# Optimization experiments

Hardware: AMD Instinct MI355X
Metric: run time of the kernel (lower is better)

Reference implementation:

```python
import jax, jax.numpy as jnp
import numpy as np

UNITS = 1024
B, T = 32, 2048


def setup_inputs() -> dict:
    key = jax.random.key(0)
    ks = jax.random.split(key, 8)
    s = 1.0 / np.sqrt(UNITS)
    return {
        "x": jax.random.normal(ks[0], (B, T, UNITS), dtype=jnp.float32),
        "hidden": jax.random.normal(ks[1], (B, UNITS), dtype=jnp.float32),
        "W1_w": jax.random.uniform(ks[2], (UNITS, UNITS), jnp.float32, -s, s),
        "W1_b": jax.random.uniform(ks[3], (UNITS,), jnp.float32, -s, s),
        "W2_w": jax.random.uniform(ks[4], (UNITS, UNITS), jnp.float32, -s, s),
        "W2_b": jax.random.uniform(ks[5], (UNITS,), jnp.float32, -s, s),
        "V_w": jax.random.uniform(ks[6], (1, UNITS), jnp.float32, -s, s),
        "V_b": jax.random.uniform(ks[7], (1,), jnp.float32, -s, s),
    }


def reference(x, hidden, W1_w, W1_b, W2_w, W2_b, V_w, V_b):
    # hidden.squeeze().unsqueeze(1): [B, U] -> [B, 1, U]
    h = hidden[:, None, :]
    # tanh(W1(x) + W2(hidden)): [B, T, U]
    att = jnp.tanh(
        jnp.einsum("btu,vu->btv", x, W1_w) + W1_b
        + jnp.einsum("bsu,vu->bsv", h, W2_w) + W2_b
    )
    # score = V(att): [B, T, 1]
    score = jnp.einsum("btu,ou->bto", att, V_w) + V_b
    # softmax over T, then squeeze().unsqueeze(1): [B, T, 1] -> [B, 1, T]
    attention_weights = jnp.swapaxes(jax.nn.softmax(score, axis=1), 1, 2)
    # bmm([B,1,T], [B,T,U]) -> [B,1,U]; squeeze().unsqueeze(0) -> [1, B, U]
    context_vector = jnp.matmul(attention_weights, x)[:, 0, :][None, :, :]
    return context_vector, attention_weights
```

## Files before the change

kernel.cpp:

```cpp
#include <hip/hip_runtime.h>
#include <hip/hip_bf16.h>
#include <cstdint>
#include <cstddef>

#define UNITS 1024
#define BDIM 32
#define TDIM 2048
#define M_TOT (BDIM*TDIM)
#define KDIM UNITS
#define NDIM UNITS
#define NPART 4

#define K2LOG2E 2.885390081777927f

typedef __attribute__((ext_vector_type(8))) short bf16x8;
typedef __attribute__((ext_vector_type(8))) unsigned short ushort8;
typedef __attribute__((ext_vector_type(4))) float f32x4;

__device__ __forceinline__ unsigned short f2bf(float f) {
  unsigned u = __float_as_uint(f);
  u += 0x7fffu + ((u >> 16) & 1u);
  return (unsigned short)(u >> 16);
}
__device__ __forceinline__ float bf2f(unsigned short h) {
  return __uint_as_float(((unsigned)h) << 16);
}

__global__ __launch_bounds__(256) void cvt_kernel(const float* __restrict__ src,
                                                  ushort* __restrict__ dst, int n8) {
  int i = blockIdx.x * blockDim.x + threadIdx.x;
  int stride = gridDim.x * blockDim.x;
  const float4* s4 = (const float4*)src;
  ushort8* d8 = (ushort8*)dst;
  for (; i < n8; i += stride) {
    float4 a = s4[2*i], b = s4[2*i+1];
    ushort8 o;
    o[0] = f2bf(a.x); o[1] = f2bf(a.y); o[2] = f2bf(a.z); o[3] = f2bf(a.w);
    o[4] = f2bf(b.x); o[5] = f2bf(b.y); o[6] = f2bf(b.z); o[7] = f2bf(b.w);
    d8[i] = o;
  }
}

__global__ __launch_bounds__(64) void prep_c_kernel(const float* __restrict__ W2w,
                                                    const float* __restrict__ hidden,
                                                    const float* __restrict__ W1b,
                                                    const float* __restrict__ W2b,
                                                    float* __restrict__ c) {
  int v = blockIdx.x;
  int l = threadIdx.x;
  float acc[BDIM];
  #pragma unroll
  for (int b = 0; b < BDIM; b++) acc[b] = 0.f;
  for (int u0 = 0; u0 < UNITS; u0 += 64) {
    float w = W2w[v*UNITS + u0 + l];
    #pragma unroll
    for (int b = 0; b < BDIM; b++) acc[b] += w * hidden[b*UNITS + u0 + l];
  }
  float bias = W1b[v] + W2b[v];
  #pragma unroll
  for (int b = 0; b < BDIM; b++) {
    float s = acc[b];
    #pragma unroll
    for (int off = 32; off > 0; off >>= 1) s += __shfl_xor(s, off);
    if (l == 0) c[b*UNITS + v] = s + bias;
  }
}

#define GLL(g, l) __builtin_amdgcn_global_load_lds(                              \
    (const __attribute__((address_space(1))) void*)(g),                          \
    (__attribute__((address_space(3))) void*)(l), 16, 0, 0)

__global__ __launch_bounds__(512, 2) void gemm_score_kernel(
    const ushort* __restrict__ A,
    const ushort* __restrict__ W,
    const float* __restrict__ c,
    const float* __restrict__ Vw,
    float* __restrict__ score)
{
  __shared__ ushort sh[2][2][16384];
  ushort* shb = &sh[0][0][0];

  const int nt = blockIdx.x & 3;
  const int m0 = (blockIdx.x >> 2) * 256;
  const int n0 = nt * 256;
  const int bb = m0 >> 11;
  const int tid = threadIdx.x;
  const int wave = tid >> 6;
  const int l = tid & 63;
  const int lrow = l & 15;
  const int lq = l >> 4;
  const int wm = (wave >> 2) * 128;
  const int wn = (wave & 3) * 64;

  const int srow = tid >> 3;
  const int s_g  = ((tid & 7) - srow) & 7;
  const int p0 = ((lq + lrow) & 7) * 8;
  const int p1 = ((lq + lrow + 4) & 7) * 8;
  const int aoff = (wm + lrow) * 64;
  const int boff = (wn + lrow) * 64;

  const ushort* gA0 = A + (size_t)(m0 + srow) * KDIM + s_g * 8;
  const ushort* gA1 = gA0 + (size_t)64 * KDIM;
  const ushort* gA2 = gA0 + (size_t)128 * KDIM;
  const ushort* gA3 = gA0 + (size_t)192 * KDIM;
  const ushort* gB0 = W + (size_t)(n0 + srow) * KDIM + s_g * 8;
  const ushort* gB1 = gB0 + (size_t)64 * KDIM;
  const ushort* gB2 = gB0 + (size_t)128 * KDIM;
  const ushort* gB3 = gB0 + (size_t)192 * KDIM;

  f32x4 acc[8][4];
  #pragma unroll
  for (int i = 0; i < 8; i++)
    #pragma unroll
    for (int j = 0; j < 4; j++) acc[i][j] = (f32x4)0.f;

  auto STAGE = [&](int buf) {
    ushort* dA = shb + buf * 32768 + wave * 512;
    ushort* dB = dA + 16384;
    GLL(gA0, dA);          GLL(gA1, dA + 4096);
    GLL(gA2, dA + 8192);   GLL(gA3, dA + 12288);
    GLL(gB0, dB);          GLL(gB1, dB + 4096);
    GLL(gB2, dB + 8192);   GLL(gB3, dB + 12288);
    gA0 += 64; gA1 += 64; gA2 += 64; gA3 += 64;
    gB0 += 64; gB1 += 64; gB2 += 64; gB3 += 64;
  };

  auto COMPUTE = [&](int buf) {
    const ushort* Ab = shb + buf * 32768;
    const ushort* Bb = Ab + 16384;
    {
      bf16x8 a[8], b[4];
      #pragma unroll
      for (int i = 0; i < 8; i++) a[i] = *(const bf16x8*)(Ab + aoff + i * 1024 + p0);
      #pragma unroll
      for (int j = 0; j < 4; j++) b[j] = *(const bf16x8*)(Bb + boff + j * 1024 + p0);
      __builtin_amdgcn_s_setprio(1);
      #pragma unroll
      for (int i = 0; i < 8; i++)
        #pragma unroll
        for (int j = 0; j < 4; j++)
          acc[i][j] = __builtin_amdgcn_mfma_f32_16x16x32_bf16(a[i], b[j], acc[i][j], 0, 0, 0);
      __builtin_amdgcn_s_setprio(0);
    }
    {
      bf16x8 a[8], b[4];
      #pragma unroll
      for (int i = 0; i < 8; i++) a[i] = *(const bf16x8*)(Ab + aoff + i * 1024 + p1);
      #pragma unroll
      for (int j = 0; j < 4; j++) b[j] = *(const bf16x8*)(Bb + boff + j * 1024 + p1);
      __builtin_amdgcn_s_setprio(1);
      #pragma unroll
      for (int i = 0; i < 8; i++)
        #pragma unroll
        for (int j = 0; j < 4; j++)
          acc[i][j] = __builtin_amdgcn_mfma_f32_16x16x32_bf16(a[i], b[j], acc[i][j], 0, 0, 0);
      __builtin_amdgcn_s_setprio(0);
    }
  };

  STAGE(0);
  STAGE(1);
  asm volatile("s_waitcnt vmcnt(8)" ::: "memory");
  __builtin_amdgcn_s_barrier();
  int cur = 0;
  #pragma unroll 1
  for (int kt = 0; kt < 14; ++kt) {
    COMPUTE(cur);
    asm volatile("s_waitcnt lgkmcnt(0)" ::: "memory");
    __builtin_amdgcn_s_barrier();
    STAGE(cur);
    asm volatile("s_waitcnt vmcnt(8)" ::: "memory");
    __builtin_amdgcn_s_barrier();
    cur ^= 1;
  }
  COMPUTE(cur);
  asm volatile("s_waitcnt lgkmcnt(0)" ::: "memory");
  __builtin_amdgcn_s_barrier();
  asm volatile("s_waitcnt vmcnt(0)" ::: "memory");
  __builtin_amdgcn_s_barrier();
  COMPUTE(cur ^ 1);

  float vw4[4], ck4[4];
  float vws = 0.f;
  #pragma unroll
  for (int j = 0; j < 4; j++) {
    int n = n0 + wn + j * 16 + lrow;
    float v = Vw[n];
    vw4[j] = v;
    vws += v;
    ck4[j] = c[bb * NDIM + n] * K2LOG2E;
  }
  float sacc[8][4];
  #pragma unroll
  for (int i = 0; i < 8; i++)
    #pragma unroll
    for (int r = 0; r < 4; r++) sacc[i][r] = 0.f;
  #pragma unroll
  for (int i = 0; i < 8; i++)
    #pragma unroll
    for (int j = 0; j < 4; j++)
      #pragma unroll
      for (int r = 0; r < 4; r++) {
        float t = __builtin_fmaf(acc[i][j][r], K2LOG2E, ck4[j]);
        float e = __builtin_amdgcn_exp2f(t);
        float rr = __builtin_amdgcn_rcpf(e + 1.f);
        sacc[i][r] = __builtin_fmaf(vw4[j], rr, sacc[i][r]);
      }

  float* sred = (float*)shb;
  #pragma unroll
  for (int i = 0; i < 8; i++)
    #pragma unroll
    for (int r = 0; r < 4; r++) {
      float s = vws - 2.f * sacc[i][r];
      s += __shfl_xor(s, 1);
      s += __shfl_xor(s, 2);
      s += __shfl_xor(s, 4);
      s += __shfl_xor(s, 8);
      if (lrow == 0) sred[wave * 128 + i * 16 + lq * 4 + r] = s;
    }
  __syncthreads();
  if (tid < 256) {
    int mh = tid >> 7;
    int ml = tid & 127;
    float v = sred[mh * 512 + ml] + sred[mh * 512 + 128 + ml]
            + sred[mh * 512 + 256 + ml] + sred[mh * 512 + 384 + ml];
    score[(size_t)nt * M_TOT + m0 + tid] = v;
  }
}

__global__ __launch_bounds__(256) void softmax_kernel(float* __restrict__ sc,
                                                      float* __restrict__ wout) {
  const int b = blockIdx.x;
  const int tid = threadIdx.x;
  float4* s4 = (float4*)(sc + (size_t)b * TDIM);
  float4 v0 = s4[2*tid], v1 = s4[2*tid+1];
  #pragma unroll
  for (int k = 1; k < NPART; k++) {
    const float4* p4 = (const float4*)(sc + (size_t)k * M_TOT + (size_t)b * TDIM);
    float4 u0 = p4[2*tid], u1 = p4[2*tid+1];
    v0.x += u0.x; v0.y += u0.y; v0.z += u0.z; v0.w += u0.w;
    v1.x += u1.x; v1.y += u1.y; v1.z += u1.z; v1.w += u1.w;
  }
  float mx = fmaxf(fmaxf(fmaxf(v0.x,v0.y),fmaxf(v0.z,v0.w)),
                   fmaxf(fmaxf(v1.x,v1.y),fmaxf(v1.z,v1.w)));
  #pragma unroll
  for (int off = 32; off > 0; off >>= 1) mx = fmaxf(mx, __shfl_xor(mx, off));
  __shared__ float redm[4];
  __shared__ float reds[4];
  if ((tid & 63) == 0) redm[tid >> 6] = mx;
  __syncthreads();
  mx = fmaxf(fmaxf(redm[0], redm[1]), fmaxf(redm[2], redm[3]));
  v0.x = __expf(v0.x - mx); v0.y = __expf(v0.y - mx);
  v0.z = __expf(v0.z - mx); v0.w = __expf(v0.w - mx);
  v1.x = __expf(v1.x - mx); v1.y = __expf(v1.y - mx);
  v1.z = __expf(v1.z - mx); v1.w = __expf(v1.w - mx);
  float sum = v0.x+v0.y+v0.z+v0.w+v1.x+v1.y+v1.z+v1.w;
  #pragma unroll
  for (int off = 32; off > 0; off >>= 1) sum += __shfl_xor(sum, off);
  if ((tid & 63) == 0) reds[tid >> 6] = sum;
  __syncthreads();
  sum = reds[0]+reds[1]+reds[2]+reds[3];
  float inv = 1.f / sum;
  v0.x *= inv; v0.y *= inv; v0.z *= inv; v0.w *= inv;
  v1.x *= inv; v1.y *= inv; v1.z *= inv; v1.w *= inv;
  s4[2*tid] = v0; s4[2*tid+1] = v1;
  float4* w4 = (float4*)(wout + (size_t)b * TDIM);
  w4[2*tid] = v0; w4[2*tid+1] = v1;
}

__global__ __launch_bounds__(256) void context_kernel(const ushort* __restrict__ xb,
                                                      const float* __restrict__ wgt,
                                                      float* __restrict__ ctx) {
  const int uc = blockIdx.x;
  const int b = blockIdx.y;
  const int tid = threadIdx.x;
  __shared__ float wl[TDIM];
  {
    const float4* wsrc = (const float4*)(wgt + (size_t)b * TDIM);
    float4* wdst = (float4*)wl;
    wdst[tid] = wsrc[tid];
    wdst[tid + 256] = wsrc[tid + 256];
  }
  __syncthreads();
  const int ut = tid & 15;
  const int tr = tid >> 4;
  const ushort* xp = xb + (size_t)b * TDIM * UNITS + uc * 128 + ut * 8;
  float a8[8];
  #pragma unroll
  for (int e = 0; e < 8; e++) a8[e] = 0.f;
  for (int t = tr; t < TDIM; t += 64) {
    ushort8 x0 = *(const ushort8*)(xp + (size_t)(t     ) * UNITS);
    ushort8 x1 = *(const ushort8*)(xp + (size_t)(t + 16) * UNITS);
    ushort8 x2 = *(const ushort8*)(xp + (size_t)(t + 32) * UNITS);
    ushort8 x3 = *(const ushort8*)(xp + (size_t)(t + 48) * UNITS);
    float w0 = wl[t], w1 = wl[t+16], w2 = wl[t+32], w3 = wl[t+48];
    #pragma unroll
    for (int e = 0; e < 8; e++) {
      a8[e] += w0 * bf2f(x0[e]);
      a8[e] += w1 * bf2f(x1[e]);
      a8[e] += w2 * bf2f(x2[e]);
      a8[e] += w3 * bf2f(x3[e]);
    }
  }
  #pragma unroll
  for (int e = 0; e < 8; e++) {
    a8[e] += __shfl_xor(a8[e], 16);
    a8[e] += __shfl_xor(a8[e], 32);
  }
  __shared__ float red[512];
  const int wave = tid >> 6;
  const int l = tid & 63;
  if (l < 16) {
    #pragma unroll
    for (int e = 0; e < 8; e++) red[wave * 128 + l * 8 + e] = a8[e];
  }
  __syncthreads();
  if (tid < 128) {
    float v = red[tid] + red[128 + tid] + red[256 + tid] + red[384 + tid];
    ctx[(size_t)b * UNITS + uc * 128 + tid] = v;
  }
}

extern "C" void kernel_launch(void* const* d_in, const int* in_sizes, int n_in,
                              void* d_out, int out_size, void* d_ws, size_t ws_size,
                              hipStream_t stream) {
  const float* x   = (const float*)d_in[0];
  const float* hid = (const float*)d_in[1];
  const float* W1w = (const float*)d_in[2];
  const float* W1b = (const float*)d_in[3];
  const float* W2w = (const float*)d_in[4];
  const float* W2b = (const float*)d_in[5];
  const float* Vw  = (const float*)d_in[6];
  float* out = (float*)d_out;

  char* ws = (char*)d_ws;
  ushort* xb   = (ushort*)ws;
  ushort* w1b  = (ushort*)(ws + (size_t)M_TOT*KDIM*2);
  float*  cbuf = (float*)(ws + (size_t)M_TOT*KDIM*2 + (size_t)NDIM*KDIM*2);
  float*  score= (float*)((char*)cbuf + (size_t)BDIM*NDIM*4);

  cvt_kernel<<<4096, 256, 0, stream>>>(x, xb, M_TOT*KDIM/8);
  cvt_kernel<<<512, 256, 0, stream>>>(W1w, w1b, NDIM*KDIM/8);
  prep_c_kernel<<<NDIM, 64, 0, stream>>>(W2w, hid, W1b, W2b, cbuf);
  gemm_score_kernel<<<M_TOT/256 * NPART, 512, 0, stream>>>(xb, w1b, cbuf, Vw, score);
  softmax_kernel<<<BDIM, 256, 0, stream>>>(score, out + (size_t)BDIM*UNITS);
  context_kernel<<<dim3(8, BDIM), 256, 0, stream>>>(xb, score, out);
}
```

Measured before the change: 579.0 us.

## Restructure GEMM mainloop into 4-slot K=32 ring with interleaved staging

Replaces the double-buffered K=64 tile pipeline with a four-slot ring of K=32 half-tiles. Each K-step is split into phases that issue async global-to-LDS loads for a future half-tile between the LDS fragment reads and the MFMA block, with per-phase barriers and vmcnt waits. The LDS swizzle is changed to match the 32-wide rows. The goal is finer-grained overlap of memory traffic with MFMA work, at the cost of more barriers per iteration and more intricate wait-count bookkeeping.

```diff
diff --git a/kernel.cpp b/kernel.cpp
--- a/kernel.cpp
+++ b/kernel.cpp
@@ -77,8 +77,7 @@
     const float* __restrict__ Vw,
     float* __restrict__ score)
 {
-  __shared__ ushort sh[2][2][16384];
-  ushort* shb = &sh[0][0][0];
+  __shared__ ushort shb[65536];
 
   const int nt = blockIdx.x & 3;
   const int m0 = (blockIdx.x >> 2) * 256;
@@ -92,21 +91,13 @@
   const int wm = (wave >> 2) * 128;
   const int wn = (wave & 3) * 64;
 
-  const int srow = tid >> 3;
-  const int s_g  = ((tid & 7) - srow) & 7;
-  const int p0 = ((lq + lrow) & 7) * 8;
-  const int p1 = ((lq + lrow + 4) & 7) * 8;
-  const int aoff = (wm + lrow) * 64;
-  const int boff = (wn + lrow) * 64;
-
-  const ushort* gA0 = A + (size_t)(m0 + srow) * KDIM + s_g * 8;
-  const ushort* gA1 = gA0 + (size_t)64 * KDIM;
-  const ushort* gA2 = gA0 + (size_t)128 * KDIM;
-  const ushort* gA3 = gA0 + (size_t)192 * KDIM;
-  const ushort* gB0 = W + (size_t)(n0 + srow) * KDIM + s_g * 8;
-  const ushort* gB1 = gB0 + (size_t)64 * KDIM;
-  const ushort* gB2 = gB0 + (size_t)128 * KDIM;
-  const ushort* gB3 = gB0 + (size_t)192 * KDIM;
+  const int s_g = ((tid & 3) - (tid >> 3)) & 3;
+  const ushort* sA = A + (size_t)(m0 + (tid >> 2)) * KDIM + s_g * 8;
+  const ushort* sB = W + (size_t)(n0 + (tid >> 2)) * KDIM + s_g * 8;
+
+  const int prot = (lq + (lrow >> 1)) & 3;
+  const int a_off = (wm + lrow) * 32 + prot * 8;
+  const int b_off = (wn + lrow) * 32 + prot * 8;
 
   f32x4 acc[8][4];
   #pragma unroll
@@ -114,71 +105,76 @@
     #pragma unroll
     for (int j = 0; j < 4; j++) acc[i][j] = (f32x4)0.f;
 
-  auto STAGE = [&](int buf) {
-    ushort* dA = shb + buf * 32768 + wave * 512;
-    ushort* dB = dA + 16384;
-    GLL(gA0, dA);          GLL(gA1, dA + 4096);
-    GLL(gA2, dA + 8192);   GLL(gA3, dA + 12288);
-    GLL(gB0, dB);          GLL(gB1, dB + 4096);
-    GLL(gB2, dB + 8192);   GLL(gB3, dB + 12288);
-    gA0 += 64; gA1 += 64; gA2 += 64; gA3 += 64;
-    gB0 += 64; gB1 += 64; gB2 += 64; gB3 += 64;
-  };
-
-  auto COMPUTE = [&](int buf) {
-    const ushort* Ab = shb + buf * 32768;
-    const ushort* Bb = Ab + 16384;
-    {
-      bf16x8 a[8], b[4];
-      #pragma unroll
-      for (int i = 0; i < 8; i++) a[i] = *(const bf16x8*)(Ab + aoff + i * 1024 + p0);
-      #pragma unroll
-      for (int j = 0; j < 4; j++) b[j] = *(const bf16x8*)(Bb + boff + j * 1024 + p0);
-      __builtin_amdgcn_s_setprio(1);
-      #pragma unroll
-      for (int i = 0; i < 8; i++)
-        #pragma unroll
-        for (int j = 0; j < 4; j++)
-          acc[i][j] = __builtin_amdgcn_mfma_f32_16x16x32_bf16(a[i], b[j], acc[i][j], 0, 0, 0);
-      __builtin_amdgcn_s_setprio(0);
-    }
-    {
-      bf16x8 a[8], b[4];
-      #pragma unroll
-      for (int i = 0; i < 8; i++) a[i] = *(const bf16x8*)(Ab + aoff + i * 1024 + p1);
-      #pragma unroll
-      for (int j = 0; j < 4; j++) b[j] = *(const bf16x8*)(Bb + boff + j * 1024 + p1);
-      __builtin_amdgcn_s_setprio(1);
-      #pragma unroll
-      for (int i = 0; i < 8; i++)
-        #pragma unroll
-        for (int j = 0; j < 4; j++)
-          acc[i][j] = __builtin_amdgcn_mfma_f32_16x16x32_bf16(a[i], b[j], acc[i][j], 0, 0, 0);
-      __builtin_amdgcn_s_setprio(0);
-    }
-  };
-
-  STAGE(0);
-  STAGE(1);
+  #define STAGE_A(TAU, C) {                                                     \
+    const ushort* g_ = sA + (TAU) * 64 + (C) * 32;                              \
+    ushort* d_ = shb + ((2*(TAU)+(C)) & 3) * 8192 + wave * 512;                 \
+    GLL(g_, d_);                                                                \
+    GLL(g_ + (size_t)128 * KDIM, d_ + 4096); }
+  #define STAGE_B(TAU, C) {                                                     \
+    const ushort* g_ = sB + (TAU) * 64 + (C) * 32;                              \
+    ushort* d_ = shb + 32768 + ((2*(TAU)+(C)) & 3) * 8192 + wave * 512;         \
+    GLL(g_, d_);                                                                \
+    GLL(g_ + (size_t)128 * KDIM, d_ + 4096); }
+
+  bf16x8 bv[4];
+
+  #define PHASE(TAU, C, IH, VM, DO_ST, ST_TAU, ST_C) {                          \
+    const int aslot_ = ((2*(TAU)+(C)) & 3) * 8192;                              \
+    const int bslot_ = 32768 + aslot_;                                          \
+    bf16x8 av[4];                                                               \
+    if ((IH) == 0) {                                                            \
+      _Pragma("unroll")                                                         \
+      for (int j = 0; j < 4; j++)                                               \
+        bv[j] = *(const bf16x8*)(shb + bslot_ + b_off + j * 512);               \
+    }                                                                           \
+    _Pragma("unroll")                                                           \
+    for (int i = 0; i < 4; i++)                                                 \
+      av[i] = *(const bf16x8*)(shb + aslot_ + a_off + ((IH)*4 + i) * 512);      \
+    if ((DO_ST) == 1) STAGE_A(ST_TAU, ST_C);                                    \
+    if ((DO_ST) == 2) STAGE_B(ST_TAU, ST_C);                                    \
+    __builtin_amdgcn_s_barrier();                                               \
+    __builtin_amdgcn_s_setprio(1);                                              \
+    _Pragma("unroll")                                                           \
+    for (int i = 0; i < 4; i++)                                                 \
+      _Pragma("unroll")                                                         \
+      for (int j = 0; j < 4; j++)                                               \
+        acc[(IH)*4 + i][j] =                                                    \
+          __builtin_amdgcn_mfma_f32_16x16x32_bf16(av[i], bv[j],                 \
+                                                  acc[(IH)*4 + i][j], 0, 0, 0); \
+    __builtin_amdgcn_s_setprio(0);                                              \
+    if ((VM) == 8) asm volatile("s_waitcnt vmcnt(8)" ::: "memory");             \
+    if ((VM) == 4) asm volatile("s_waitcnt vmcnt(4)" ::: "memory");             \
+    if ((VM) == 0) asm volatile("s_waitcnt vmcnt(0)" ::: "memory");             \
+    __builtin_amdgcn_s_barrier();                                               \
+    __builtin_amdgcn_sched_barrier(0);                                          \
+  }
+
+  STAGE_A(0, 0); STAGE_B(0, 0);
+  STAGE_A(0, 1); STAGE_B(0, 1);
+  STAGE_A(1, 0); STAGE_B(1, 0);
   asm volatile("s_waitcnt vmcnt(8)" ::: "memory");
   __builtin_amdgcn_s_barrier();
-  int cur = 0;
+  __builtin_amdgcn_sched_barrier(0);
+
   #pragma unroll 1
-  for (int kt = 0; kt < 14; ++kt) {
-    COMPUTE(cur);
-    asm volatile("s_waitcnt lgkmcnt(0)" ::: "memory");
-    __builtin_amdgcn_s_barrier();
-    STAGE(cur);
-    asm volatile("s_waitcnt vmcnt(8)" ::: "memory");
-    __builtin_amdgcn_s_barrier();
-    cur ^= 1;
-  }
-  COMPUTE(cur);
-  asm volatile("s_waitcnt lgkmcnt(0)" ::: "memory");
-  __builtin_amdgcn_s_barrier();
-  asm volatile("s_waitcnt vmcnt(0)" ::: "memory");
-  __builtin_amdgcn_s_barrier();
-  COMPUTE(cur ^ 1);
+  for (int tau = 0; tau < 14; ++tau) {
+    PHASE(tau, 0, 0, -1, 1, tau + 1, 1);
+    PHASE(tau, 0, 1,  8, 2, tau + 1, 1);
+    PHASE(tau, 1, 0, -1, 1, tau + 2, 0);
+    PHASE(tau, 1, 1,  8, 2, tau + 2, 0);
+  }
+  PHASE(14, 0, 0, -1, 1, 15, 1);
+  PHASE(14, 0, 1,  8, 2, 15, 1);
+  PHASE(14, 1, 0, -1, 0, 0, 0);
+  PHASE(14, 1, 1,  4, 0, 0, 0);
+  PHASE(15, 0, 0, -1, 0, 0, 0);
+  PHASE(15, 0, 1,  0, 0, 0, 0);
+  PHASE(15, 1, 0, -1, 0, 0, 0);
+  PHASE(15, 1, 1, -1, 0, 0, 0);
+
+  #undef PHASE
+  #undef STAGE_A
+  #undef STAGE_B
 
   float vw4[4], ck4[4];
   float vws = 0.f;
```

After: 562.8 us. 1.03x faster.
